# Performance work log

Measured on AMD Instinct MI355X. Metric: run time of the kernel, lower is better.

Reference implementation:

```python
import jax, jax.numpy as jnp
import numpy as np

EMB_DIM = 512
HIDDEN = 512
VOCAB = 50257
SEQ_LEN = 1024
IMG_H = 32
IMG_W = 32
ATTN_OUT = 64


def setup_inputs() -> dict:
    key = jax.random.key(0)
    ks = jax.random.split(key, 8)
    s_emb = 1.0 / np.sqrt(EMB_DIM)
    s_h = 1.0 / np.sqrt(HIDDEN)
    return {
        "instructions_batch": jax.random.randint(ks[0], (1, SEQ_LEN), 0, VOCAB, dtype=jnp.int64 if jax.config.jax_enable_x64 else jnp.int32),
        "emb_table": jax.random.normal(ks[1], (VOCAB, EMB_DIM), jnp.float32),
        "w_ih": jax.random.uniform(ks[2], (4 * HIDDEN, EMB_DIM), jnp.float32, -s_h, s_h),
        "w_hh": jax.random.uniform(ks[3], (4 * HIDDEN, HIDDEN), jnp.float32, -s_h, s_h),
        "b_ih": jax.random.uniform(ks[4], (4 * HIDDEN,), jnp.float32, -s_h, s_h),
        "b_hh": jax.random.uniform(ks[5], (4 * HIDDEN,), jnp.float32, -s_h, s_h),
        "attn_w": jax.random.uniform(ks[6], (ATTN_OUT, HIDDEN), jnp.float32, -s_emb, s_emb),
        "attn_b": jnp.zeros((ATTN_OUT,), jnp.float32),
    }


def _lstm_encode(tokens, emb_table, w_ih, w_hh, b_ih, b_hh):
    # tokens: [S] int; embeddings gathered once, then scan the recurrence.
    xs = emb_table[tokens]                      # [S, E]
    x_gates = xs @ w_ih.T + (b_ih + b_hh)       # [S, 4H] precompute input contribution

    def step(carry, xg):
        h, c = carry                            # [H], [H]
        gates = xg + h @ w_hh.T                 # [4H]
        i, f, g, o = jnp.split(gates, 4)
        i = jax.nn.sigmoid(i)
        f = jax.nn.sigmoid(f)
        g = jnp.tanh(g)
        o = jax.nn.sigmoid(o)
        c = f * c + i * g
        h = o * jnp.tanh(c)
        return (h, c), None

    h0 = jnp.zeros((HIDDEN,), xs.dtype)
    (h, _), _ = jax.lax.scan(step, (h0, h0), x_gates)
    return h                                     # [H]


def reference(instructions_batch, emb_table, w_ih, w_hh, b_ih, b_hh, attn_w, attn_b):
    h = _lstm_encode(instructions_batch[0], emb_table, w_ih, w_hh, b_ih, b_hh)
    x_instr_rep = h[None, :]                                    # [1, H]
    attn = jax.nn.sigmoid(x_instr_rep @ attn_w.T + attn_b)      # [1, 64]
    x_attention = jnp.broadcast_to(attn[:, :, None, None], (1, ATTN_OUT, IMG_H, IMG_W))
    return (x_attention, x_instr_rep)
```

## Files before the change

### kernel.cpp

```cpp
#include <hip/hip_runtime.h>
#include <hip/hip_bf16.h>
#include <math.h>

#define SEQ    1024
#define EMB    512
#define HID    512
#define G4     2048
#define NBLK   32
#define UPB    16
#define NSLOT  4

typedef unsigned long long u64;

__global__ __launch_bounds__(256) void xgates_kernel(
    const int* __restrict__ tok, const float* __restrict__ emb,
    const float* __restrict__ w_ih, const float* __restrict__ b_ih,
    const float* __restrict__ b_hh, float* __restrict__ xg)
{
  __shared__ float xs[64][68];
  __shared__ float wsh[64][68];
  __shared__ int   tok_s[64];

  const int tid = threadIdx.x;
  const int r0  = (int)blockIdx.x * 64;
  const int t0  = (int)blockIdx.y * 64;

  if (tid < 64) tok_s[tid] = tok[t0 + tid];
  __syncthreads();

  const int tx = tid & 15;
  const int ty = tid >> 4;

  float acc[4][4];
#pragma unroll
  for (int i = 0; i < 4; ++i)
#pragma unroll
    for (int j = 0; j < 4; ++j) acc[i][j] = 0.f;

  for (int kc = 0; kc < EMB; kc += 64) {
#pragma unroll
    for (int it = 0; it < 4; ++it) {
      int id  = it * 256 + tid;
      int row = id >> 4;
      int c4  = id & 15;
      float4 xv = *(const float4*)(emb + (size_t)tok_s[row] * EMB + kc + c4 * 4);
      *(float4*)&xs[row][c4 * 4] = xv;
      float4 wv = *(const float4*)(w_ih + (size_t)(r0 + row) * EMB + kc + c4 * 4);
      *(float4*)&wsh[row][c4 * 4] = wv;
    }
    __syncthreads();

#pragma unroll
    for (int k4 = 0; k4 < 16; ++k4) {
      float4 xv[4], wv[4];
#pragma unroll
      for (int i = 0; i < 4; ++i) xv[i] = *(const float4*)&xs[ty * 4 + i][k4 * 4];
#pragma unroll
      for (int j = 0; j < 4; ++j) wv[j] = *(const float4*)&wsh[tx * 4 + j][k4 * 4];
#pragma unroll
      for (int i = 0; i < 4; ++i)
#pragma unroll
        for (int j = 0; j < 4; ++j) {
          acc[i][j] += xv[i].x * wv[j].x + xv[i].y * wv[j].y
                     + xv[i].z * wv[j].z + xv[i].w * wv[j].w;
        }
    }
    __syncthreads();
  }

  const int rbase = r0 + tx * 4;
  float bias[4];
#pragma unroll
  for (int j = 0; j < 4; ++j) bias[j] = b_ih[rbase + j] + b_hh[rbase + j];

#pragma unroll
  for (int i = 0; i < 4; ++i) {
    int t = t0 + ty * 4 + i;
    float4 o;
    o.x = acc[i][0] + bias[0];
    o.y = acc[i][1] + bias[1];
    o.z = acc[i][2] + bias[2];
    o.w = acc[i][3] + bias[3];
    *(float4*)(xg + (size_t)t * G4 + rbase) = o;
  }
}

__global__ __launch_bounds__(512) void lstm_scan_kernel(
    const float* __restrict__ xg, const float* __restrict__ w_hh,
    u64* hslot )
{
  __shared__ float h_lds[512];
  __shared__ float part_lds[2][8 * 64];

  const int tid = threadIdx.x;
  const int blk = blockIdx.x;
  const int w   = tid >> 6;
  const int l   = tid & 63;
  const int q   = l >> 4;
  const int jj  = l & 15;
  const int grow = q * HID + blk * UPB + jj;

  float wreg[64];
  {
    const float* wp = w_hh + (size_t)grow * HID + w * 64;
#pragma unroll
    for (int k4 = 0; k4 < 16; ++k4) {
      float4 v = ((const float4*)wp)[k4];
      wreg[4 * k4 + 0] = v.x; wreg[4 * k4 + 1] = v.y;
      wreg[4 * k4 + 2] = v.z; wreg[4 * k4 + 3] = v.w;
    }
  }

  float c_reg = 0.f;
  float xgv = (w == 0) ? xg[grow] : 0.f;

  for (int t = 0; t < SEQ; ++t) {
    u64 word;
    const u64* src = hslot + (size_t)(t & (NSLOT - 1)) * HID + tid;
    do {
      word = __hip_atomic_load(src, __ATOMIC_RELAXED, __HIP_MEMORY_SCOPE_AGENT);
    } while ((unsigned)(word >> 32) != (unsigned)t);
    h_lds[tid] = __uint_as_float((unsigned)(word & 0xffffffffu));

    const float* hb = &h_lds[w * 64];
    float p0 = 0.f, p1 = 0.f, p2 = 0.f, p3 = 0.f;
#pragma unroll
    for (int k = 0; k < 16; ++k) {
      p0 += wreg[k]      * hb[k];
      p1 += wreg[k + 16] * hb[k + 16];
      p2 += wreg[k + 32] * hb[k + 32];
      p3 += wreg[k + 48] * hb[k + 48];
    }
    part_lds[t & 1][w * 64 + l] = (p0 + p1) + (p2 + p3);
    __syncthreads();

    if (w == 0) {
      const float* pp = &part_lds[t & 1][0];
      float s = ((pp[l]       + pp[64 + l]) + (pp[128 + l] + pp[192 + l]))
              + ((pp[256 + l] + pp[320 + l]) + (pp[384 + l] + pp[448 + l]));
      float gv = s + xgv;

      int tn = (t + 1 < SEQ) ? (t + 1) : (SEQ - 1);
      xgv = xg[(size_t)tn * G4 + grow];

      float gi = __shfl(gv, jj,      64);
      float gf = __shfl(gv, jj + 16, 64);
      float gg = __shfl(gv, jj + 32, 64);
      float go = __shfl(gv, jj + 48, 64);

      if (l < UPB) {
        const float LOG2E = 1.442695041f;
        float i_ = 1.f / (1.f + __builtin_exp2f(-LOG2E * gi));
        float f_ = 1.f / (1.f + __builtin_exp2f(-LOG2E * gf));
        float g_ = 2.f / (1.f + __builtin_exp2f(-2.f * LOG2E * gg)) - 1.f;
        float o_ = 1.f / (1.f + __builtin_exp2f(-LOG2E * go));
        c_reg = f_ * c_reg + i_ * g_;
        float hv = o_ * (2.f / (1.f + __builtin_exp2f(-2.f * LOG2E * c_reg)) - 1.f);
        u64 outw = ((u64)(unsigned)(t + 1) << 32) | (u64)__float_as_uint(hv);
        __hip_atomic_store(hslot + (size_t)((t + 1) & (NSLOT - 1)) * HID + blk * UPB + jj,
                           outw, __ATOMIC_RELAXED, __HIP_MEMORY_SCOPE_AGENT);
      }
    }
  }
}

__global__ __launch_bounds__(256) void head_kernel(
    const u64* __restrict__ hpacked, const float* __restrict__ attn_w,
    const float* __restrict__ attn_b, float* __restrict__ out)
{
  __shared__ float red[4];
  __shared__ float aval;
  const int r   = blockIdx.x;
  const int tid = threadIdx.x;

  float h0 = __uint_as_float((unsigned)(hpacked[tid]       & 0xffffffffu));
  float h1 = __uint_as_float((unsigned)(hpacked[256 + tid] & 0xffffffffu));

  float p = attn_w[(size_t)r * HID + tid] * h0
          + attn_w[(size_t)r * HID + 256 + tid] * h1;
#pragma unroll
  for (int off = 1; off < 64; off <<= 1) p += __shfl_xor(p, off, 64);
  if ((tid & 63) == 0) red[tid >> 6] = p;
  __syncthreads();
  if (tid == 0) {
    float sum = red[0] + red[1] + red[2] + red[3] + attn_b[r];
    aval = 1.f / (1.f + __expf(-sum));
  }
  __syncthreads();

  float a = aval;
  float4 av = make_float4(a, a, a, a);
  ((float4*)(out + (size_t)r * 1024))[tid] = av;

  if (r == 0) {
    out[65536 + tid]       = h0;
    out[65536 + 256 + tid] = h1;
  }
}

extern "C" void kernel_launch(void* const* d_in, const int* in_sizes, int n_in,
                              void* d_out, int out_size, void* d_ws, size_t ws_size,
                              hipStream_t stream) {
  const int*   tok    = (const int*)  d_in[0];
  const float* emb    = (const float*)d_in[1];
  const float* w_ih   = (const float*)d_in[2];
  const float* w_hh   = (const float*)d_in[3];
  const float* b_ih   = (const float*)d_in[4];
  const float* b_hh   = (const float*)d_in[5];
  const float* attn_w = (const float*)d_in[6];
  const float* attn_b = (const float*)d_in[7];
  float* out = (float*)d_out;

  char* ws = (char*)d_ws;
  float* xg    = (float*)ws;
  u64*   hslot = (u64*)(ws + (size_t)SEQ * G4 * 4);

  hipMemsetAsync(hslot, 0, NSLOT * HID * sizeof(u64), stream);

  dim3 gA(G4 / 64, SEQ / 64);
  xgates_kernel<<<gA, 256, 0, stream>>>(tok, emb, w_ih, b_ih, b_hh, xg);
  lstm_scan_kernel<<<NBLK, 512, 0, stream>>>(xg, w_hh, hslot);
  head_kernel<<<64, 256, 0, stream>>>(hslot, attn_w, attn_b, out);
}
```

Before: 1.815 ms.

## Replicate LSTM scan per XCD group and exchange hidden state through group-local slots

Launches eight replicas of the 32-block recurrent scan, each group taking its id from blockIdx & 7. The intent is that each group's blocks land on one XCD and swap h through their own slot buffer, written with plain stores and polled with sc0 loads, so the per-step handoff stays in that XCD's L2 instead of agent-scope memory. Every eighth spin still falls back to the shared agent-scope slot, so the scan cannot stall if placement differs. It also reads h from LDS as float4. The cost is eight times the redundant compute and register-resident weights, and all 256 large blocks must be resident at once for the spin-wait scheme to work.

```diff
diff --git a/kernel.cpp b/kernel.cpp
--- a/kernel.cpp
+++ b/kernel.cpp
@@ -7,6 +7,7 @@
 #define HID    512
 #define G4     2048
 #define NBLK   32
+#define NGRP   8
 #define UPB    16
 #define NSLOT  4
 
@@ -87,18 +88,22 @@
 
 __global__ __launch_bounds__(512) void lstm_scan_kernel(
     const float* __restrict__ xg, const float* __restrict__ w_hh,
-    u64* hslot )
+    u64* hslot ,
+    u64* hfast )
 {
   __shared__ float h_lds[512];
   __shared__ float part_lds[2][8 * 64];
 
-  const int tid = threadIdx.x;
-  const int blk = blockIdx.x;
-  const int w   = tid >> 6;
-  const int l   = tid & 63;
-  const int q   = l >> 4;
-  const int jj  = l & 15;
-  const int grow = q * HID + blk * UPB + jj;
+  const int tid  = threadIdx.x;
+  const int gid  = (int)blockIdx.x & (NGRP - 1);
+  const int ublk = (int)blockIdx.x >> 3;
+  const int w    = tid >> 6;
+  const int l    = tid & 63;
+  const int q    = l >> 4;
+  const int jj   = l & 15;
+  const int grow = q * HID + ublk * UPB + jj;
+
+  u64* fbase = hfast + (size_t)gid * NSLOT * HID;
 
   float wreg[64];
   {
@@ -115,21 +120,39 @@
   float xgv = (w == 0) ? xg[grow] : 0.f;
 
   for (int t = 0; t < SEQ; ++t) {
+    const u64* fsrc = fbase + (size_t)(t & (NSLOT - 1)) * HID + tid;
+    const u64* ssrc = hslot + (size_t)(t & (NSLOT - 1)) * HID + tid;
     u64 word;
-    const u64* src = hslot + (size_t)(t & (NSLOT - 1)) * HID + tid;
-    do {
-      word = __hip_atomic_load(src, __ATOMIC_RELAXED, __HIP_MEMORY_SCOPE_AGENT);
-    } while ((unsigned)(word >> 32) != (unsigned)t);
+    int spins = 0;
+    while (true) {
+      asm volatile("global_load_dwordx2 %0, %1, off sc0\n\t"
+                   "s_waitcnt vmcnt(0)"
+                   : "=v"(word) : "v"(fsrc) : "memory");
+      if ((unsigned)(word >> 32) == (unsigned)t) break;
+      if (((++spins) & 7) == 0) {
+        word = __hip_atomic_load(ssrc, __ATOMIC_RELAXED, __HIP_MEMORY_SCOPE_AGENT);
+        if ((unsigned)(word >> 32) == (unsigned)t) break;
+      }
+    }
     h_lds[tid] = __uint_as_float((unsigned)(word & 0xffffffffu));
 
-    const float* hb = &h_lds[w * 64];
+    const float*  hb  = &h_lds[w * 64];
+    const float4* hb4 = (const float4*)hb;
     float p0 = 0.f, p1 = 0.f, p2 = 0.f, p3 = 0.f;
 #pragma unroll
-    for (int k = 0; k < 16; ++k) {
-      p0 += wreg[k]      * hb[k];
-      p1 += wreg[k + 16] * hb[k + 16];
-      p2 += wreg[k + 32] * hb[k + 32];
-      p3 += wreg[k + 48] * hb[k + 48];
+    for (int k4 = 0; k4 < 4; ++k4) {
+      float4 h0 = hb4[k4];
+      float4 h1 = hb4[k4 + 4];
+      float4 h2 = hb4[k4 + 8];
+      float4 h3 = hb4[k4 + 12];
+      p0 += wreg[4 * k4 + 0] * h0.x; p0 += wreg[4 * k4 + 1] * h0.y;
+      p0 += wreg[4 * k4 + 2] * h0.z; p0 += wreg[4 * k4 + 3] * h0.w;
+      p1 += wreg[16 + 4 * k4 + 0] * h1.x; p1 += wreg[16 + 4 * k4 + 1] * h1.y;
+      p1 += wreg[16 + 4 * k4 + 2] * h1.z; p1 += wreg[16 + 4 * k4 + 3] * h1.w;
+      p2 += wreg[32 + 4 * k4 + 0] * h2.x; p2 += wreg[32 + 4 * k4 + 1] * h2.y;
+      p2 += wreg[32 + 4 * k4 + 2] * h2.z; p2 += wreg[32 + 4 * k4 + 3] * h2.w;
+      p3 += wreg[48 + 4 * k4 + 0] * h3.x; p3 += wreg[48 + 4 * k4 + 1] * h3.y;
+      p3 += wreg[48 + 4 * k4 + 2] * h3.z; p3 += wreg[48 + 4 * k4 + 3] * h3.w;
     }
     part_lds[t & 1][w * 64 + l] = (p0 + p1) + (p2 + p3);
     __syncthreads();
@@ -157,7 +180,11 @@
         c_reg = f_ * c_reg + i_ * g_;
         float hv = o_ * (2.f / (1.f + __builtin_exp2f(-2.f * LOG2E * c_reg)) - 1.f);
         u64 outw = ((u64)(unsigned)(t + 1) << 32) | (u64)__float_as_uint(hv);
-        __hip_atomic_store(hslot + (size_t)((t + 1) & (NSLOT - 1)) * HID + blk * UPB + jj,
+
+        u64* fdst = fbase + (size_t)((t + 1) & (NSLOT - 1)) * HID + ublk * UPB + jj;
+        asm volatile("global_store_dwordx2 %0, %1, off"
+                     :: "v"(fdst), "v"(outw) : "memory");
+        __hip_atomic_store(hslot + (size_t)((t + 1) & (NSLOT - 1)) * HID + ublk * UPB + jj,
                            outw, __ATOMIC_RELAXED, __HIP_MEMORY_SCOPE_AGENT);
       }
     }
@@ -214,11 +241,14 @@
   char* ws = (char*)d_ws;
   float* xg    = (float*)ws;
   u64*   hslot = (u64*)(ws + (size_t)SEQ * G4 * 4);
-
-  hipMemsetAsync(hslot, 0, NSLOT * HID * sizeof(u64), stream);
+  u64*   hfast = hslot + (size_t)NSLOT * HID;
+
+  hipMemsetAsync(hslot, 0,
+                 (size_t)(NSLOT * HID + NGRP * NSLOT * HID) * sizeof(u64),
+                 stream);
 
   dim3 gA(G4 / 64, SEQ / 64);
   xgates_kernel<<<gA, 256, 0, stream>>>(tok, emb, w_ih, b_ih, b_hh, xg);
-  lstm_scan_kernel<<<NBLK, 512, 0, stream>>>(xg, w_hh, hslot);
+  lstm_scan_kernel<<<NBLK * NGRP, 512, 0, stream>>>(xg, w_hh, hslot, hfast);
   head_kernel<<<64, 256, 0, stream>>>(hslot, attn_w, attn_b, out);
 }
```

New measurement: 2.600 ms. 43.2% more time.
